# Kernel optimization log

Measured on AMD Instinct MI355X. Metric: run time of the kernel, lower is better.

## Reference

```python
import jax, jax.numpy as jnp
import numpy as np

N, F_IN, F_OUT = 8192, 256, 256
ALPHA = 0.2  # LeakyReLU negative slope
NEG = -9e15

def setup_inputs() -> dict:
    key = jax.random.key(0)
    k1, k2, k3, k4, k5 = jax.random.split(key, 5)
    h = jax.random.normal(k1, (N, F_IN), dtype=jnp.float32)
    adj = jax.random.randint(k2, (N, N), 0, 2, dtype=jnp.int32)
    W_w = jax.random.normal(k3, (F_IN, F_OUT), dtype=jnp.float32) / np.sqrt(F_IN)
    W_b = jax.random.normal(k4, (F_OUT,), dtype=jnp.float32) * 0.01
    a = jax.random.normal(k5, (2 * F_OUT, 1), dtype=jnp.float32) / np.sqrt(2 * F_OUT)
    return {"h": h, "adj": adj, "W_w": W_w, "W_b": W_b, "a": a}

def reference(h, adj, W_w, W_b, a):
    # Wh: [N, F_OUT]
    Wh = h @ W_w + W_b
    a1 = a[:F_OUT, 0]   # scores for source node i (row)
    a2 = a[F_OUT:, 0]   # scores for target node j (col)
    # e[i,j] = leakyrelu(Wh_i . a1 + Wh_j . a2)  -- separable form of the
    # original repeat/cat construction, identical math without the NxNx2F tensor.
    e = jax.nn.leaky_relu((Wh @ a1)[:, None] + (Wh @ a2)[None, :], negative_slope=ALPHA)
    attention = jnp.where(adj > 0, e, NEG)
    attention = jax.nn.softmax(attention, axis=1)
    # dropout is identity in eval / p=0
    h_prime = attention @ Wh  # [N, F_OUT]
    return h_prime
```

## Files before the change

kernel.cpp:

```cpp
#include <hip/hip_runtime.h>
#include <stdint.h>

#define NN 8192
#define FD 256
#define LOG2E 1.44269504088896340736f
#define SPLIT 8
#define JSLICE (NN / SPLIT)
#define NIT (JSLICE / 32)

typedef __attribute__((ext_vector_type(8))) __bf16 bf16x8;
typedef __attribute__((ext_vector_type(4))) float f32x4;

__device__ __forceinline__ unsigned short f2bf(float x) {
    unsigned u = __float_as_uint(x);
    u = u + 0x7fffu + ((u >> 16) & 1u);
    return (unsigned short)(u >> 16);
}
__device__ __forceinline__ bf16x8 ld_bf8(const unsigned short* p) {
    uint4 v = *(const uint4*)p;
    return __builtin_bit_cast(bf16x8, v);
}
__device__ __forceinline__ unsigned pack_trunc2(float a, float b) {
    return __builtin_amdgcn_perm(__float_as_uint(b), __float_as_uint(a), 0x07060302u);
}

__global__ __launch_bounds__(256) void wtrans_kernel(const float* __restrict__ W,
                                                     unsigned short* __restrict__ WbT) {
    int idx = blockIdx.x * 256 + threadIdx.x;
    int k = idx >> 8, f = idx & 255;
    WbT[f * 256 + k] = f2bf(W[idx]);
}

__global__ __launch_bounds__(256) void adjpack_kernel(const int* __restrict__ adj,
                                                      unsigned* __restrict__ adjB) {
    int t = threadIdx.x;
    int l = t & 63, w = t >> 6;
    int i = blockIdx.x * 4 + w;
    const int* arow = adj + (size_t)i * NN;
    unsigned* brow = adjB + (size_t)i * (NN / 32);
    #pragma unroll 2
    for (int c = 0; c < 32; ++c) {
        int base = c * 256;
        int v0 = arow[base + l];
        int v1 = arow[base + 64 + l];
        int v2 = arow[base + 128 + l];
        int v3 = arow[base + 192 + l];
        unsigned long long b0 = __ballot(v0 > 0);
        unsigned long long b1 = __ballot(v1 > 0);
        unsigned long long b2 = __ballot(v2 > 0);
        unsigned long long b3 = __ballot(v3 > 0);
        if (l == 0) {
            uint4 lo = make_uint4((unsigned)b0, (unsigned)(b0 >> 32),
                                  (unsigned)b1, (unsigned)(b1 >> 32));
            uint4 hi = make_uint4((unsigned)b2, (unsigned)(b2 >> 32),
                                  (unsigned)b3, (unsigned)(b3 >> 32));
            *(uint4*)(brow + c * 8) = lo;
            *(uint4*)(brow + c * 8 + 4) = hi;
        }
    }
}

__global__ __launch_bounds__(256) void btrans_kernel(const unsigned* __restrict__ rm,
                                                     unsigned* __restrict__ tm) {
    __shared__ unsigned tile[64 * 65];
    int t = threadIdx.x;
    int l = t & 63, r0 = t >> 6;
    int i0 = (blockIdx.x & 127) * 64;
    int w0 = (blockIdx.x >> 7) * 64;
    #pragma unroll
    for (int k = 0; k < 16; ++k) {
        int r = k * 4 + r0;
        tile[r * 65 + l] = rm[(size_t)(i0 + r) * (NN / 32) + w0 + l];
    }
    __syncthreads();
    #pragma unroll
    for (int k = 0; k < 16; ++k) {
        int wi = k * 4 + r0;
        tm[(size_t)(w0 + wi) * NN + i0 + l] = tile[l * 65 + wi];
    }
}

__global__ __launch_bounds__(256) void gemm1_kernel(const float* __restrict__ h,
                                                    const unsigned short* __restrict__ WbT,
                                                    const float* __restrict__ bias,
                                                    const float* __restrict__ av,
                                                    unsigned short* __restrict__ PBu,
                                                    float* __restrict__ f1p,
                                                    float* __restrict__ f2p) {
    __shared__ float Wh_s[256 * 33];
    __shared__ float red_s[2 * 8 * 32];
    int t = threadIdx.x;
    int l = t & 63, w = t >> 6;
    int i0 = blockIdx.x * 32;
    int fbase = w * 64;
    int cl = l & 15, q = l >> 4;

    f32x4 acc[2][4] = {};
    const float* hA0 = h + (size_t)(i0 + cl) * FD;
    const float* hA1 = h + (size_t)(i0 + 16 + cl) * FD;

    #pragma unroll
    for (int ks = 0; ks < 8; ++ks) {
        int kk = ks * 32 + q * 8;
        union { unsigned short u[8]; bf16x8 v; } ua0, ua1;
        float4 x0 = *(const float4*)(hA0 + kk);
        float4 x1 = *(const float4*)(hA0 + kk + 4);
        float4 y0 = *(const float4*)(hA1 + kk);
        float4 y1 = *(const float4*)(hA1 + kk + 4);
        ua0.u[0]=f2bf(x0.x); ua0.u[1]=f2bf(x0.y); ua0.u[2]=f2bf(x0.z); ua0.u[3]=f2bf(x0.w);
        ua0.u[4]=f2bf(x1.x); ua0.u[5]=f2bf(x1.y); ua0.u[6]=f2bf(x1.z); ua0.u[7]=f2bf(x1.w);
        ua1.u[0]=f2bf(y0.x); ua1.u[1]=f2bf(y0.y); ua1.u[2]=f2bf(y0.z); ua1.u[3]=f2bf(y0.w);
        ua1.u[4]=f2bf(y1.x); ua1.u[5]=f2bf(y1.y); ua1.u[6]=f2bf(y1.z); ua1.u[7]=f2bf(y1.w);
        #pragma unroll
        for (int bg = 0; bg < 4; ++bg) {
            bf16x8 bF = ld_bf8(WbT + (fbase + bg * 16 + cl) * 256 + kk);
            acc[0][bg] = __builtin_amdgcn_mfma_f32_16x16x32_bf16(ua0.v, bF, acc[0][bg], 0, 0, 0);
            acc[1][bg] = __builtin_amdgcn_mfma_f32_16x16x32_bf16(ua1.v, bF, acc[1][bg], 0, 0, 0);
        }
    }

    #pragma unroll
    for (int mt = 0; mt < 2; ++mt)
        #pragma unroll
        for (int bg = 0; bg < 4; ++bg)
            #pragma unroll
            for (int e = 0; e < 4; ++e) {
                int il = mt * 16 + q * 4 + e;
                int fl = fbase + bg * 16 + cl;
                Wh_s[fl * 33 + il] = acc[mt][bg][e] + bias[fl];
            }
    __syncthreads();
    {
        size_t jcBase = (size_t)blockIdx.x * 8192;
        #pragma unroll
        for (int u = 0; u < 4; ++u) {
            int fg = u * 4 + (t >> 6);
            int ll = t & 63;
            int c2 = ll & 15, q2 = ll >> 4;
            const float* src = &Wh_s[(fg * 16 + c2) * 33 + q2 * 8];
            union { unsigned short us[8]; uint4 v; } p;
            #pragma unroll
            for (int e = 0; e < 8; ++e) p.us[e] = f2bf(src[e]);
            *(uint4*)(PBu + jcBase + fg * 512 + ll * 8) = p.v;
        }
    }
    {
        int i = t & 31, fc = t >> 5;
        float s1 = 0.f, s2 = 0.f;
        #pragma unroll
        for (int fo = 0; fo < 32; ++fo) {
            int f = fc * 32 + fo;
            float wv = Wh_s[f * 33 + i];
            s1 += wv * av[f];
            s2 += wv * av[256 + f];
        }
        red_s[fc * 32 + i] = s1;
        red_s[256 + fc * 32 + i] = s2;
    }
    __syncthreads();
    if (t < 32) {
        float s = 0.f;
        #pragma unroll
        for (int fc = 0; fc < 8; ++fc) s += red_s[fc * 32 + t];
        f1p[i0 + t] = s * LOG2E;
    } else if (t < 64) {
        int i = t - 32;
        float s = 0.f;
        #pragma unroll
        for (int fc = 0; fc < 8; ++fc) s += red_s[256 + fc * 32 + i];
        f2p[i0 + i] = s * LOG2E;
    }
}

__global__ __launch_bounds__(256, 2) void gat_kernel(const unsigned* __restrict__ adjBT,
                                                     const unsigned short* __restrict__ PBu,
                                                     const float* __restrict__ f1p,
                                                     const float* __restrict__ f2p,
                                                     float* __restrict__ num,
                                                     float* __restrict__ den) {
    __shared__ unsigned mask_s[NIT * 128];
    __shared__ float f2_s[JSLICE];

    int t = threadIdx.x;
    int l = t & 63, w = t >> 6;
    int strip = blockIdx.x & 63;
    int s = blockIdx.x >> 6;
    int i0b = strip * 128;
    int j0 = s * JSLICE;
    int jw0 = j0 / 32;
    int cl = l & 15, q = l >> 4;

    #pragma unroll
    for (int c = 0; c < 16; ++c) {
        int idx = c * 256 + t;
        int jt = idx >> 7, rl = idx & 127;
        mask_s[idx] = adjBT[(size_t)(jw0 + jt) * NN + i0b + rl];
    }
    *(float4*)&f2_s[t * 4] = *(const float4*)(f2p + j0 + t * 4);
    __syncthreads();

    int rA = w * 32 + cl;
    float f1vA = f1p[i0b + rA];
    float f1vB = f1p[i0b + rA + 16];
    const unsigned short* pb = PBu + (size_t)jw0 * 8192 + l * 8;

    f32x4 accA[16] = {}, accB[16] = {};
    float rsA = 0.f, rsB = 0.f;

    #pragma unroll 1
    for (int jt = 0; jt < NIT; ++jt) {
        bf16x8 B[16];
        const unsigned short* pbj = pb + (size_t)jt * 8192;
        #pragma unroll
        for (int fg = 0; fg < 16; ++fg) B[fg] = ld_bf8(pbj + fg * 512);

        unsigned mwA = mask_s[jt * 128 + rA];
        unsigned mwB = mask_s[jt * 128 + rA + 16];
        float4 F0 = *(const float4*)&f2_s[jt * 32 + q * 8];
        float4 F1 = *(const float4*)&f2_s[jt * 32 + q * 8 + 4];

        unsigned bA = mwA >> (q * 8), bB = mwB >> (q * 8);
        float fe[8] = {F0.x, F0.y, F0.z, F0.w, F1.x, F1.y, F1.z, F1.w};
        float wA[8], wB[8];
        #pragma unroll
        for (int e = 0; e < 8; ++e) {
            float sA = f1vA + fe[e];
            sA = fmaxf(sA, 0.2f * sA);
            float xA = __builtin_amdgcn_exp2f(sA);
            xA = (bA >> e) & 1 ? xA : 0.f;
            rsA += xA; wA[e] = xA;
            float sB = f1vB + fe[e];
            sB = fmaxf(sB, 0.2f * sB);
            float xB = __builtin_amdgcn_exp2f(sB);
            xB = (bB >> e) & 1 ? xB : 0.f;
            rsB += xB; wB[e] = xB;
        }
        union { unsigned u[4]; bf16x8 v; } afA, afB;
        afA.u[0] = pack_trunc2(wA[0], wA[1]); afA.u[1] = pack_trunc2(wA[2], wA[3]);
        afA.u[2] = pack_trunc2(wA[4], wA[5]); afA.u[3] = pack_trunc2(wA[6], wA[7]);
        afB.u[0] = pack_trunc2(wB[0], wB[1]); afB.u[1] = pack_trunc2(wB[2], wB[3]);
        afB.u[2] = pack_trunc2(wB[4], wB[5]); afB.u[3] = pack_trunc2(wB[6], wB[7]);

        #pragma unroll
        for (int fg = 0; fg < 16; ++fg) {
            accA[fg] = __builtin_amdgcn_mfma_f32_16x16x32_bf16(afA.v, B[fg], accA[fg], 0, 0, 0);
            accB[fg] = __builtin_amdgcn_mfma_f32_16x16x32_bf16(afB.v, B[fg], accB[fg], 0, 0, 0);
        }
    }

    rsA += __shfl_xor(rsA, 16); rsA += __shfl_xor(rsA, 32);
    rsB += __shfl_xor(rsB, 16); rsB += __shfl_xor(rsB, 32);
    if (l < 16) {
        den[(size_t)s * NN + i0b + w * 32 + l] = rsA;
        den[(size_t)s * NN + i0b + w * 32 + 16 + l] = rsB;
    }

    float* nrow = num + (size_t)s * NN * FD;
    #pragma unroll
    for (int e = 0; e < 4; ++e) {
        int r0 = i0b + w * 32 + q * 4 + e;
        #pragma unroll
        for (int fg = 0; fg < 16; ++fg) {
            nrow[(size_t)r0 * FD + fg * 16 + cl] = accA[fg][e];
            nrow[(size_t)(r0 + 16) * FD + fg * 16 + cl] = accB[fg][e];
        }
    }
}

__global__ __launch_bounds__(256) void combine_kernel(const float* __restrict__ num,
                                                      const float* __restrict__ den,
                                                      float* __restrict__ out) {
    int idx = blockIdx.x * 256 + threadIdx.x;
    int i = idx >> 8;
    float nsum = 0.f, dsum = 0.f;
    #pragma unroll
    for (int s = 0; s < SPLIT; ++s) {
        nsum += num[(size_t)s * NN * FD + idx];
        dsum += den[(size_t)s * NN + i];
    }
    out[idx] = nsum / dsum;
}

extern "C" void kernel_launch(void* const* d_in, const int* in_sizes, int n_in,
                              void* d_out, int out_size, void* d_ws, size_t ws_size,
                              hipStream_t stream) {
    const float* h   = (const float*)d_in[0];
    const int*   adj = (const int*)d_in[1];
    const float* W   = (const float*)d_in[2];
    const float* b   = (const float*)d_in[3];
    const float* a   = (const float*)d_in[4];
    float* out = (float*)d_out;

    char* ws = (char*)d_ws;
    unsigned short* PBu = (unsigned short*)ws;
    unsigned short* WbT = (unsigned short*)(ws + (4u << 20));
    float* f1p = (float*)(ws + (4u << 20) + (128u << 10));
    float* f2p = f1p + NN;
    float* den = f2p + NN;
    unsigned* adjB  = (unsigned*)(ws + (8u << 20));
    unsigned* adjBT = (unsigned*)(ws + (16u << 20));
    float* num = (float*)(ws + (24u << 20));

    adjpack_kernel<<<NN / 4, 256, 0, stream>>>(adj, adjB);
    wtrans_kernel<<<256, 256, 0, stream>>>(W, WbT);
    btrans_kernel<<<512, 256, 0, stream>>>(adjB, adjBT);
    gemm1_kernel<<<256, 256, 0, stream>>>(h, WbT, b, a, PBu, f1p, f2p);
    gat_kernel<<<64 * SPLIT, 256, 0, stream>>>(adjBT, PBu, f1p, f2p, num, den);
    combine_kernel<<<NN * FD / 256, 256, 0, stream>>>(num, den, out);
}
```

Measured before the change: 485.7 us.

## Stage B tiles in LDS via async double-buffered loads, halve rows per block

The GAT kernel now streams the bf16 value matrix into shared memory using asynchronous global-to-LDS loads with a double buffer. Each wave reads B fragments from LDS instead of holding 16 register fragments loaded straight from global memory. Rows per block drop from 128 to 64 and the grid doubles, which cuts accumulator registers per wave and should raise occupancy and overlap loads with MFMA. The cost is twice as many blocks re-reading the same B slice from L2, plus a block-wide barrier every two tiles.

```diff
diff --git a/kernel.cpp b/kernel.cpp
--- a/kernel.cpp
+++ b/kernel.cpp
@@ -7,6 +7,7 @@
 #define SPLIT 8
 #define JSLICE (NN / SPLIT)
 #define NIT (JSLICE / 32)
+#define NPH (NIT / 2)
 
 typedef __attribute__((ext_vector_type(8))) __bf16 bf16x8;
 typedef __attribute__((ext_vector_type(4))) float f32x4;
@@ -22,6 +23,11 @@
 }
 __device__ __forceinline__ unsigned pack_trunc2(float a, float b) {
     return __builtin_amdgcn_perm(__float_as_uint(b), __float_as_uint(a), 0x07060302u);
+}
+__device__ __forceinline__ void async_ld16(const void* g, void* lds) {
+    __builtin_amdgcn_global_load_lds(
+        (const __attribute__((address_space(1))) void*)g,
+        (__attribute__((address_space(3))) void*)lds, 16, 0, 0);
 }
 
 __global__ __launch_bounds__(256) void wtrans_kernel(const float* __restrict__ W,
@@ -178,92 +184,94 @@
                                                      const float* __restrict__ f2p,
                                                      float* __restrict__ num,
                                                      float* __restrict__ den) {
-    __shared__ unsigned mask_s[NIT * 128];
+    __shared__ __align__(16) unsigned short Bs[2][2 * 8192];
+    __shared__ unsigned mask_s[NIT * 64];
     __shared__ float f2_s[JSLICE];
 
     int t = threadIdx.x;
     int l = t & 63, w = t >> 6;
-    int strip = blockIdx.x & 63;
-    int s = blockIdx.x >> 6;
-    int i0b = strip * 128;
+    int strip = blockIdx.x & 127;
+    int s = blockIdx.x >> 7;
+    int i0b = strip * 64;
     int j0 = s * JSLICE;
     int jw0 = j0 / 32;
     int cl = l & 15, q = l >> 4;
 
     #pragma unroll
-    for (int c = 0; c < 16; ++c) {
+    for (int c = 0; c < 8; ++c) {
         int idx = c * 256 + t;
-        int jt = idx >> 7, rl = idx & 127;
+        int jt = idx >> 6, rl = idx & 63;
         mask_s[idx] = adjBT[(size_t)(jw0 + jt) * NN + i0b + rl];
     }
     *(float4*)&f2_s[t * 4] = *(const float4*)(f2p + j0 + t * 4);
-    __syncthreads();
-
-    int rA = w * 32 + cl;
-    float f1vA = f1p[i0b + rA];
-    float f1vB = f1p[i0b + rA + 16];
-    const unsigned short* pb = PBu + (size_t)jw0 * 8192 + l * 8;
-
-    f32x4 accA[16] = {}, accB[16] = {};
-    float rsA = 0.f, rsB = 0.f;
+
+    const char* pbBase = (const char*)(PBu + (size_t)jw0 * 8192);
+    #pragma unroll
+    for (int k = 0; k < 8; ++k)
+        async_ld16(pbBase + k * 4096 + t * 16, (char*)&Bs[0][0] + k * 4096 + t * 16);
+
+    int rowi = i0b + w * 16 + cl;
+    float f1v = f1p[rowi];
+
+    f32x4 acc[16] = {};
+    float rs = 0.f;
 
     #pragma unroll 1
-    for (int jt = 0; jt < NIT; ++jt) {
-        bf16x8 B[16];
-        const unsigned short* pbj = pb + (size_t)jt * 8192;
-        #pragma unroll
-        for (int fg = 0; fg < 16; ++fg) B[fg] = ld_bf8(pbj + fg * 512);
-
-        unsigned mwA = mask_s[jt * 128 + rA];
-        unsigned mwB = mask_s[jt * 128 + rA + 16];
-        float4 F0 = *(const float4*)&f2_s[jt * 32 + q * 8];
-        float4 F1 = *(const float4*)&f2_s[jt * 32 + q * 8 + 4];
-
-        unsigned bA = mwA >> (q * 8), bB = mwB >> (q * 8);
-        float fe[8] = {F0.x, F0.y, F0.z, F0.w, F1.x, F1.y, F1.z, F1.w};
-        float wA[8], wB[8];
-        #pragma unroll
-        for (int e = 0; e < 8; ++e) {
-            float sA = f1vA + fe[e];
-            sA = fmaxf(sA, 0.2f * sA);
-            float xA = __builtin_amdgcn_exp2f(sA);
-            xA = (bA >> e) & 1 ? xA : 0.f;
-            rsA += xA; wA[e] = xA;
-            float sB = f1vB + fe[e];
-            sB = fmaxf(sB, 0.2f * sB);
-            float xB = __builtin_amdgcn_exp2f(sB);
-            xB = (bB >> e) & 1 ? xB : 0.f;
-            rsB += xB; wB[e] = xB;
-        }
-        union { unsigned u[4]; bf16x8 v; } afA, afB;
-        afA.u[0] = pack_trunc2(wA[0], wA[1]); afA.u[1] = pack_trunc2(wA[2], wA[3]);
-        afA.u[2] = pack_trunc2(wA[4], wA[5]); afA.u[3] = pack_trunc2(wA[6], wA[7]);
-        afB.u[0] = pack_trunc2(wB[0], wB[1]); afB.u[1] = pack_trunc2(wB[2], wB[3]);
-        afB.u[2] = pack_trunc2(wB[4], wB[5]); afB.u[3] = pack_trunc2(wB[6], wB[7]);
-
-        #pragma unroll
-        for (int fg = 0; fg < 16; ++fg) {
-            accA[fg] = __builtin_amdgcn_mfma_f32_16x16x32_bf16(afA.v, B[fg], accA[fg], 0, 0, 0);
-            accB[fg] = __builtin_amdgcn_mfma_f32_16x16x32_bf16(afB.v, B[fg], accB[fg], 0, 0, 0);
-        }
-    }
-
-    rsA += __shfl_xor(rsA, 16); rsA += __shfl_xor(rsA, 32);
-    rsB += __shfl_xor(rsB, 16); rsB += __shfl_xor(rsB, 32);
-    if (l < 16) {
-        den[(size_t)s * NN + i0b + w * 32 + l] = rsA;
-        den[(size_t)s * NN + i0b + w * 32 + 16 + l] = rsB;
-    }
+    for (int ph = 0; ph < NPH; ++ph) {
+        __syncthreads();
+        if (ph + 1 < NPH) {
+            const char* src = pbBase + (size_t)(2 * ph + 2) * 16384;
+            char* dst = (char*)&Bs[(ph + 1) & 1][0];
+            #pragma unroll
+            for (int k = 0; k < 8; ++k)
+                async_ld16(src + k * 4096 + t * 16, dst + k * 4096 + t * 16);
+        }
+        const unsigned short* bb = &Bs[ph & 1][0];
+        #pragma unroll
+        for (int u = 0; u < 2; ++u) {
+            int jt = 2 * ph + u;
+            unsigned mw = mask_s[jt * 64 + w * 16 + cl];
+            float4 F0 = *(const float4*)&f2_s[jt * 32 + q * 8];
+            float4 F1 = *(const float4*)&f2_s[jt * 32 + q * 8 + 4];
+
+            unsigned bits = mw >> (q * 8);
+            float fe[8] = {F0.x, F0.y, F0.z, F0.w, F1.x, F1.y, F1.z, F1.w};
+            float wv[8];
+            #pragma unroll
+            for (int e = 0; e < 8; ++e) {
+                float sv = f1v + fe[e];
+                sv = fmaxf(sv, 0.2f * sv);
+                float x = __builtin_amdgcn_exp2f(sv);
+                x = (bits >> e) & 1 ? x : 0.f;
+                rs += x;
+                wv[e] = x;
+            }
+            union { unsigned uu[4]; bf16x8 v; } af;
+            af.uu[0] = pack_trunc2(wv[0], wv[1]);
+            af.uu[1] = pack_trunc2(wv[2], wv[3]);
+            af.uu[2] = pack_trunc2(wv[4], wv[5]);
+            af.uu[3] = pack_trunc2(wv[6], wv[7]);
+
+            const unsigned short* bu = bb + u * 8192 + l * 8;
+            #pragma unroll
+            for (int fg = 0; fg < 16; ++fg) {
+                bf16x8 B = ld_bf8(bu + fg * 512);
+                acc[fg] = __builtin_amdgcn_mfma_f32_16x16x32_bf16(af.v, B, acc[fg], 0, 0, 0);
+            }
+        }
+    }
+
+    rs += __shfl_xor(rs, 16);
+    rs += __shfl_xor(rs, 32);
+    if (l < 16) den[(size_t)s * NN + i0b + w * 16 + l] = rs;
 
     float* nrow = num + (size_t)s * NN * FD;
     #pragma unroll
     for (int e = 0; e < 4; ++e) {
-        int r0 = i0b + w * 32 + q * 4 + e;
-        #pragma unroll
-        for (int fg = 0; fg < 16; ++fg) {
-            nrow[(size_t)r0 * FD + fg * 16 + cl] = accA[fg][e];
-            nrow[(size_t)(r0 + 16) * FD + fg * 16 + cl] = accB[fg][e];
-        }
+        int r = i0b + w * 16 + q * 4 + e;
+        #pragma unroll
+        for (int fg = 0; fg < 16; ++fg)
+            nrow[(size_t)r * FD + fg * 16 + cl] = acc[fg][e];
     }
 }
 
@@ -305,6 +313,6 @@
     wtrans_kernel<<<256, 256, 0, stream>>>(W, WbT);
     btrans_kernel<<<512, 256, 0, stream>>>(adjB, adjBT);
     gemm1_kernel<<<256, 256, 0, stream>>>(h, WbT, b, a, PBu, f1p, f2p);
-    gat_kernel<<<64 * SPLIT, 256, 0, stream>>>(adjBT, PBu, f1p, f2p, num, den);
+    gat_kernel<<<128 * SPLIT, 256, 0, stream>>>(adjBT, PBu, f1p, f2p, num, den);
     combine_kernel<<<NN * FD / 256, 256, 0, stream>>>(num, den, out);
 }
```

New measurement: 456.9 us. 5.9% less time.
